# Optimization experiments

Hardware: AMD Instinct MI355X
Metric: run time of the kernel (lower is better)

The kernel has to match this reference:

```python
import jax, jax.numpy as jnp
import numpy as np

HIDDEN = 256


def setup_inputs() -> dict:
    key = jax.random.key(0)
    ks = jax.random.split(key, 16)
    bs, T, wv, vocab, inp = 256, 256, 100, 600, 64
    s = 0.05
    lengths = jax.random.randint(ks[2], (bs,), 2, T + 1)
    lengths = lengths.at[0].set(T)  # ensure max(decoder_length) == T-1
    return {
        "encoder_out": jax.random.normal(ks[0], (bs, inp), jnp.float32),
        "encoded_captions": jax.random.normal(ks[1], (bs, T, wv), jnp.float32),
        "w_ih": jax.random.normal(ks[3], (4 * HIDDEN, inp), jnp.float32) * s,
        "w_hh": jax.random.normal(ks[4], (4 * HIDDEN, HIDDEN), jnp.float32) * s,
        "b_ih": jax.random.normal(ks[5], (4 * HIDDEN,), jnp.float32) * s,
        "b_hh": jax.random.normal(ks[6], (4 * HIDDEN,), jnp.float32) * s,
        "W_out": jax.random.normal(ks[7], (vocab, HIDDEN), jnp.float32) * s,
        "b_out": jax.random.normal(ks[8], (vocab,), jnp.float32) * s,
        "W_emb": jax.random.normal(ks[9], (inp, wv), jnp.float32) * s,
        "b_emb": jax.random.normal(ks[10], (inp,), jnp.float32) * s,
        "W_h": jax.random.normal(ks[11], (HIDDEN, inp), jnp.float32) * s,
        "b_h": jax.random.normal(ks[12], (HIDDEN,), jnp.float32) * s,
        "W_c": jax.random.normal(ks[13], (HIDDEN, inp), jnp.float32) * s,
        "b_c": jax.random.normal(ks[14], (HIDDEN,), jnp.float32) * s,
        "caption_lengths": lengths,
    }


def reference(encoder_out, encoded_captions, w_ih, w_hh, b_ih, b_hh,
              W_out, b_out, W_emb, b_emb, W_h, b_h, W_c, b_c,
              caption_lengths):
    # sort by descending caption length (as torch.sort(descending=True))
    sort_idx = jnp.argsort(-caption_lengths)
    lengths = caption_lengths[sort_idx]
    enc = encoder_out[sort_idx]                  # [bs, 64]
    caps = encoded_captions[sort_idx]            # [bs, T, 100]

    h0 = enc @ W_h.T + b_h                       # [bs, H]
    c0 = enc @ W_c.T + b_c                       # [bs, H]
    emb = caps @ W_emb.T + b_emb                 # [bs, T, 64]

    dec_len = lengths - 1                        # [bs]
    steps = caps.shape[1] - 1                    # == max(dec_len) by construction
    xs = jnp.swapaxes(emb[:, :steps], 0, 1)      # [steps, bs, 64]
    ts = jnp.arange(steps)

    def step(carry, inp):
        h, c = carry
        x, t = inp
        gates = x @ w_ih.T + b_ih + h @ w_hh.T + b_hh      # [bs, 4H]
        i, f, g, o = jnp.split(gates, 4, axis=-1)           # torch gate order i,f,g,o
        i = jax.nn.sigmoid(i); f = jax.nn.sigmoid(f)
        g = jnp.tanh(g);       o = jax.nn.sigmoid(o)
        c_new = f * c + i * g
        h_new = o * jnp.tanh(c_new)
        active = (t < dec_len)[:, None]                     # shrinking batch == mask (sorted)
        logits = h_new @ W_out.T + b_out                    # [bs, vocab]
        pred = jnp.where(active, logits, jnp.float32(-1.0))
        h = jnp.where(active, h_new, h)
        c = jnp.where(active, c_new, c)
        return (h, c), pred

    (_, _), preds = jax.lax.scan(step, (h0, c0), (xs, ts))
    predicts = jnp.swapaxes(preds, 0, 1)         # [bs, steps, vocab]
    return predicts, caps, dec_len, sort_idx
```

## Files before the change

### kernel.cpp

```cpp
#include <hip/hip_runtime.h>
#include <hip/hip_fp16.h>

#define BS 256
#define T 256
#define STEPS 255
#define WV 100
#define INP 64
#define H 256
#define G4 1024
#define VOCAB 600
#define VT 38

typedef _Float16 f16x2 __attribute__((ext_vector_type(2)));
typedef _Float16 f16x8 __attribute__((ext_vector_type(8)));
typedef float f32x4 __attribute__((ext_vector_type(4)));

__device__ __forceinline__ float fdot2(unsigned w, unsigned h, float acc) {
#if defined(__has_builtin) && __has_builtin(__builtin_amdgcn_fdot2)
    return __builtin_amdgcn_fdot2(__builtin_bit_cast(f16x2, w),
                                  __builtin_bit_cast(f16x2, h), acc, false);
#else
    __half2 wv = *(const __half2*)&w;
    __half2 hv = *(const __half2*)&h;
    float2 wf = __half22float2(wv), hf = __half22float2(hv);
    return acc + wf.x * hf.x + wf.y * hf.y;
#endif
}

__device__ __forceinline__ float quad_reduce(float x) {
    int a = __builtin_bit_cast(int, x);
    int b = __builtin_amdgcn_update_dpp(0, a, 0xB1, 0xF, 0xF, true);
    float s = x + __builtin_bit_cast(float, b);
    int c = __builtin_bit_cast(int, s);
    int d = __builtin_amdgcn_update_dpp(0, c, 0x4E, 0xF, 0xF, true);
    return s + __builtin_bit_cast(float, d);
}

__device__ __forceinline__ f32x4 mfma16(uint4 a, uint4 b, f32x4 c) {
    return __builtin_amdgcn_mfma_f32_16x16x32_f16(
        __builtin_bit_cast(f16x8, a), __builtin_bit_cast(f16x8, b), c, 0, 0, 0);
}

__global__ void k_sort(const int* __restrict__ lens, int* __restrict__ sidx,
                       int* __restrict__ dlen, float* __restrict__ out_dec,
                       float* __restrict__ out_sidx) {
    __shared__ int L[BS];
    int i = threadIdx.x;
    L[i] = lens[i];
    __syncthreads();
    int li = L[i];
    int r = 0;
    for (int j = 0; j < BS; ++j) {
        int lj = L[j];
        r += (lj > li) || (lj == li && j < i);
    }
    sidx[r] = i;
    dlen[r] = li - 1;
    out_sidx[r] = (float)i;
    out_dec[r]  = (float)(li - 1);
}

__global__ void k_gather(const float* __restrict__ cin, const int* __restrict__ sidx,
                         float* __restrict__ cout) {
    int b = blockIdx.x;
    int src = sidx[b];
    const float4* in  = (const float4*)(cin + (size_t)src * T * WV);
    float4* out       = (float4*)(cout + (size_t)b * T * WV);
    for (int i = threadIdx.x; i < T * WV / 4; i += 256) out[i] = in[i];
}

__global__ void k_wcomb(const float* __restrict__ w_ih, const float* __restrict__ W_emb,
                        float* __restrict__ Wc) {
    int idx = blockIdx.x * 256 + threadIdx.x;
    int r = idx / WV, cc = idx % WV;
    float acc = 0.f;
    for (int k = 0; k < INP; ++k) acc += w_ih[r * INP + k] * W_emb[k * WV + cc];
    Wc[idx] = acc;
}

__global__ void k_bcomb(const float* __restrict__ w_ih, const float* __restrict__ b_ih,
                        const float* __restrict__ b_hh, const float* __restrict__ b_emb,
                        float* __restrict__ bc) {
    int r = blockIdx.x * 256 + threadIdx.x;
    float acc = b_ih[r] + b_hh[r];
    for (int k = 0; k < INP; ++k) acc += w_ih[r * INP + k] * b_emb[k];
    bc[r] = acc;
}

__global__ void k_packw(const float* __restrict__ w_hh, __half2* __restrict__ wR) {
    int idx = blockIdx.x * 256 + threadIdx.x;
    wR[idx] = __floats2half2_rn(w_hh[(size_t)idx * 2], w_hh[(size_t)idx * 2 + 1]);
}

__global__ void k_packwo(const float* __restrict__ Wo, __half* __restrict__ woHi,
                         __half* __restrict__ woLo) {
    int idx = blockIdx.x * 256 + threadIdx.x;
    int fi = idx >> 9;
    int l  = (idx >> 3) & 63;
    int j  = idx & 7;
    int vt = fi >> 3, kt = fi & 7;
    int v = vt * 16 + (l & 15);
    int k = kt * 32 + ((l >> 4) << 3) + j;
    float w = (v < VOCAB) ? Wo[(size_t)v * H + k] : 0.f;
    __half hi = __float2half(w);
    __half lo = __float2half(w - __half2float(hi));
    woHi[idx] = hi;
    woLo[idx] = lo;
}

__global__ void k_packcaps(const float* __restrict__ caps, __half* __restrict__ cHi,
                           __half* __restrict__ cLo) {
    int idx = blockIdx.x * 256 + threadIdx.x;
    int k = idx & 127;
    int bt = idx >> 7;
    float v = (k < WV) ? caps[(size_t)bt * WV + k] : 0.f;
    __half hi = __float2half(v);
    cHi[idx] = hi;
    cLo[idx] = __float2half(v - __half2float(hi));
}

__global__ void k_packwc(const float* __restrict__ Wc, __half* __restrict__ wcHi,
                         __half* __restrict__ wcLo) {
    int idx = blockIdx.x * 256 + threadIdx.x;
    int fi = idx >> 9;
    int l  = (idx >> 3) & 63;
    int j  = idx & 7;
    int nt = fi >> 2, kt = fi & 3;
    int n = nt * 16 + (l & 15);
    int k = kt * 32 + ((l >> 4) << 3) + j;
    float w = (k < WV) ? Wc[(size_t)n * WV + k] : 0.f;
    __half hi = __float2half(w);
    wcHi[idx] = hi;
    wcLo[idx] = __float2half(w - __half2float(hi));
}

__global__ void k_inithc(const float* __restrict__ enc, const int* __restrict__ sidx,
                         const float* __restrict__ W_h, const float* __restrict__ b_h,
                         const float* __restrict__ W_c, const float* __restrict__ b_c,
                         float* __restrict__ h_st, float* __restrict__ c_st) {
    int b = blockIdx.x, j = threadIdx.x;
    __shared__ __align__(16) float e[INP];
    int src = sidx[b];
    if (j < INP) e[j] = enc[src * INP + j];
    __syncthreads();
    const float4* e4  = (const float4*)e;
    const float4* wh4 = (const float4*)(W_h + (size_t)j * INP);
    const float4* wc4 = (const float4*)(W_c + (size_t)j * INP);
    float ah = b_h[j], ac = b_c[j];
    #pragma unroll
    for (int k4 = 0; k4 < INP / 4; ++k4) {
        float4 ev = e4[k4];
        float4 wh = wh4[k4];
        float4 wc = wc4[k4];
        ah += ev.x * wh.x + ev.y * wh.y + ev.z * wh.z + ev.w * wh.w;
        ac += ev.x * wc.x + ev.y * wc.y + ev.z * wc.z + ev.w * wc.w;
    }
    h_st[b * H + j] = ah;
    c_st[b * H + j] = ac;
}

__global__ __launch_bounds__(256) void k_xg(const __half* __restrict__ cHi,
        const __half* __restrict__ cLo, const __half* __restrict__ wcHi,
        const __half* __restrict__ wcLo, const float* __restrict__ bc,
        const int* __restrict__ dlen, float* __restrict__ xg, int t0, int Cc) {
    int b = blockIdx.y;
    int ct0 = blockIdx.x * 32;
    if (t0 + ct0 >= dlen[b]) return;
    int tid = threadIdx.x;
    int l = tid & 63, wid = tid >> 6;
    int lhi = l >> 4, llo = l & 15;

    uint4 aH[2][4], aL[2][4];
    #pragma unroll
    for (int m = 0; m < 2; ++m) {
        int rr = ct0 + m * 16 + llo;
        if (rr >= Cc) rr = Cc - 1;
        size_t base = ((size_t)b * T + (t0 + rr)) * 128 + lhi * 8;
        #pragma unroll
        for (int kt = 0; kt < 4; ++kt) {
            aH[m][kt] = *(const uint4*)(cHi + base + kt * 32);
            aL[m][kt] = *(const uint4*)(cLo + base + kt * 32);
        }
    }
    const uint4* bh4 = (const uint4*)wcHi;
    const uint4* bl4 = (const uint4*)wcLo;
    for (int i = 0; i < 16; ++i) {
        int nt = wid * 16 + i;
        float bias = bc[nt * 16 + llo];
        f32x4 acc0 = {bias, bias, bias, bias};
        f32x4 acc1 = acc0;
        #pragma unroll
        for (int kt = 0; kt < 4; ++kt) {
            uint4 bh = bh4[(nt * 4 + kt) * 64 + l];
            uint4 bl = bl4[(nt * 4 + kt) * 64 + l];
            acc0 = mfma16(aH[0][kt], bh, acc0);
            acc1 = mfma16(aH[1][kt], bh, acc1);
            acc0 = mfma16(aH[0][kt], bl, acc0);
            acc1 = mfma16(aH[1][kt], bl, acc1);
            acc0 = mfma16(aL[0][kt], bh, acc0);
            acc1 = mfma16(aL[1][kt], bh, acc1);
        }
        #pragma unroll
        for (int m = 0; m < 2; ++m) {
            f32x4 A = m ? acc1 : acc0;
            #pragma unroll
            for (int ii = 0; ii < 4; ++ii) {
                int rr = ct0 + m * 16 + lhi * 4 + ii;
                if (rr < Cc)
                    xg[((size_t)b * Cc + rr) * G4 + nt * 16 + llo] = A[ii];
            }
        }
    }
}

#define LSTM_SMEM (131072 + 2 * 1152)

__global__ __launch_bounds__(512)
__attribute__((amdgpu_waves_per_eu(2, 2)))
void k_lstm(const __half2* __restrict__ wR,
        const float* __restrict__ xg, const int* __restrict__ dlen,
        float* __restrict__ h_st, float* __restrict__ c_st,
        __half* __restrict__ hck, int t0, int Cc) {
    extern __shared__ __align__(16) char smem[];
    uint4*    wl4  = (uint4*)smem;
    unsigned* hbuf = (unsigned*)(smem + 131072);

    int b = blockIdx.x, tid = threadIdx.x;
    int steps_b = dlen[b];
    if (t0 >= steps_b) return;

    int lane = tid & 63;
    int q = lane & 3;
    int Q = tid >> 2;
    int rx = 2 * Q + (q & 1);

    const uint4* wR4 = (const uint4*)wR;

    uint4 wreg[6][8];
    #pragma unroll
    for (int j = 0; j < 6; ++j) {
        int grow = (j >> 1) * 256 + 2 * Q + (j & 1);
        #pragma unroll
        for (int u = 0; u < 8; ++u)
            wreg[j][u] = wR4[grow * 32 + q * 8 + u];
    }
    #pragma unroll
    for (int s = 0; s < 2; ++s)
        #pragma unroll
        for (int u = 0; u < 8; ++u)
            wl4[((u * 2 + s) * 128 + Q) * 4 + q] =
                wR4[(768 + 2 * Q + s) * 32 + q * 8 + u];

    float c = c_st[b * H + rx];
    float hcur = h_st[b * H + rx];
    {
        __half hh16 = __float2half(hcur);
        __half hl16 = __float2half(hcur - __half2float(hh16));
        if (q < 2) {
            int hidx = (rx >> 6) * 72 + (rx & 63);
            ((__half*)(hbuf))[hidx] = hh16;
            ((__half*)(hbuf + 144))[hidx] = hl16;
        }
    }
    __syncthreads();

    int tend = t0 + Cc; if (tend > steps_b) tend = steps_b;
    const float* xgp = xg + (size_t)b * Cc * G4;
    __half* hckp = hck + (size_t)b * Cc * H;
    int p = 0;

    for (int t = t0; t < tend; ++t) {
        float xi = xgp[rx];
        float xf = xgp[256 + rx];
        float xgg = xgp[512 + rx];
        float xo = xgp[768 + rx];

        const uint4* hh4 = (const uint4*)(hbuf + p * 288);
        const uint4* hl4 = (const uint4*)(hbuf + p * 288 + 144);

        float ah[8], al[8];
        #pragma unroll
        for (int j = 0; j < 8; ++j) { ah[j] = 0.f; al[j] = 0.f; }

        #pragma unroll
        for (int u = 0; u < 8; ++u) {
            uint4 hh = hh4[q * 9 + u];
            uint4 hl = hl4[q * 9 + u];
            #pragma unroll
            for (int j = 0; j < 6; ++j) {
                uint4 w = wreg[j][u];
                ah[j] = fdot2(w.x, hh.x, ah[j]);
                ah[j] = fdot2(w.y, hh.y, ah[j]);
                ah[j] = fdot2(w.z, hh.z, ah[j]);
                ah[j] = fdot2(w.w, hh.w, ah[j]);
                al[j] = fdot2(w.x, hl.x, al[j]);
                al[j] = fdot2(w.y, hl.y, al[j]);
                al[j] = fdot2(w.z, hl.z, al[j]);
                al[j] = fdot2(w.w, hl.w, al[j]);
            }
            uint4 w6 = wl4[((u * 2 + 0) * 128 + Q) * 4 + q];
            uint4 w7 = wl4[((u * 2 + 1) * 128 + Q) * 4 + q];
            ah[6] = fdot2(w6.x, hh.x, ah[6]);
            ah[6] = fdot2(w6.y, hh.y, ah[6]);
            ah[6] = fdot2(w6.z, hh.z, ah[6]);
            ah[6] = fdot2(w6.w, hh.w, ah[6]);
            al[6] = fdot2(w6.x, hl.x, al[6]);
            al[6] = fdot2(w6.y, hl.y, al[6]);
            al[6] = fdot2(w6.z, hl.z, al[6]);
            al[6] = fdot2(w6.w, hl.w, al[6]);
            ah[7] = fdot2(w7.x, hh.x, ah[7]);
            ah[7] = fdot2(w7.y, hh.y, ah[7]);
            ah[7] = fdot2(w7.z, hh.z, ah[7]);
            ah[7] = fdot2(w7.w, hh.w, ah[7]);
            al[7] = fdot2(w7.x, hl.x, al[7]);
            al[7] = fdot2(w7.y, hl.y, al[7]);
            al[7] = fdot2(w7.z, hl.z, al[7]);
            al[7] = fdot2(w7.w, hl.w, al[7]);
        }

        float tt[8];
        #pragma unroll
        for (int j = 0; j < 8; ++j) tt[j] = quad_reduce(ah[j] + al[j]);

        int odd = q & 1;
        float pi = odd ? tt[1] : tt[0];
        float pf = odd ? tt[3] : tt[2];
        float pg = odd ? tt[5] : tt[4];
        float po = odd ? tt[7] : tt[6];
        float iv = 1.f / (1.f + __expf(-(pi + xi)));
        float fv = 1.f / (1.f + __expf(-(pf + xf)));
        float gv = tanhf(pg + xgg);
        float ov = 1.f / (1.f + __expf(-(po + xo)));
        c = fv * c + iv * gv;
        float nh = ov * tanhf(c);
        hcur = nh;
        __half hh16 = __float2half(nh);
        __half hl16 = __float2half(nh - __half2float(hh16));
        if (q < 2) {
            hckp[rx] = hh16;
            int hidx = (rx >> 6) * 72 + (rx & 63);
            ((__half*)(hbuf + (p ^ 1) * 288))[hidx] = hh16;
            ((__half*)(hbuf + (p ^ 1) * 288 + 144))[hidx] = hl16;
        }
        __syncthreads();
        p ^= 1;
        xgp += G4;
        hckp += H;
    }
    if (q < 2) { h_st[b * H + rx] = hcur; c_st[b * H + rx] = c; }
}

__global__ __launch_bounds__(64) void k_logits(const __half* __restrict__ hck,
        const __half* __restrict__ woHi, const __half* __restrict__ woLo,
        const float* __restrict__ bo, const int* __restrict__ dlen,
        float* __restrict__ pred, int t0, int Cc) {
    int b = blockIdx.y;
    int ct0 = blockIdx.x * 32;
    if (ct0 >= Cc) return;
    int steps_b = dlen[b];
    int l = threadIdx.x;
    int lhi = l >> 4, llo = l & 15;

    if (t0 + ct0 >= steps_b) {
        for (int r = 0; r < 32; ++r) {
            int t = t0 + ct0 + r;
            if (r >= Cc - ct0 || t >= STEPS) break;
            float* pr = pred + ((size_t)b * STEPS + t) * VOCAB;
            for (int v = l; v < VOCAB; v += 64) pr[v] = -1.f;
        }
        return;
    }

    uint4 a[2][8];
    #pragma unroll
    for (int m = 0; m < 2; ++m) {
        int rr = ct0 + m * 16 + llo;
        int rc = (rr < Cc) ? rr : (Cc - 1);
        const uint4* rp = (const uint4*)(hck + ((size_t)b * Cc + rc) * H);
        #pragma unroll
        for (int kt = 0; kt < 8; ++kt) a[m][kt] = rp[kt * 4 + lhi];
    }

    const uint4* bh4 = (const uint4*)woHi;
    const uint4* bl4 = (const uint4*)woLo;
    for (int vt = 0; vt < VT; ++vt) {
        int v = vt * 16 + llo;
        float bias = (v < VOCAB) ? bo[v] : 0.f;
        f32x4 acc0 = {bias, bias, bias, bias};
        f32x4 acc1 = acc0;
        #pragma unroll
        for (int kt = 0; kt < 8; ++kt) {
            uint4 bh = bh4[(vt * 8 + kt) * 64 + l];
            acc0 = mfma16(a[0][kt], bh, acc0);
            acc1 = mfma16(a[1][kt], bh, acc1);
        }
        #pragma unroll
        for (int kt = 0; kt < 8; ++kt) {
            uint4 bl = bl4[(vt * 8 + kt) * 64 + l];
            acc0 = mfma16(a[0][kt], bl, acc0);
            acc1 = mfma16(a[1][kt], bl, acc1);
        }
        if (v < VOCAB) {
            #pragma unroll
            for (int m = 0; m < 2; ++m) {
                f32x4 A = m ? acc1 : acc0;
                #pragma unroll
                for (int i = 0; i < 4; ++i) {
                    int r = ct0 + m * 16 + lhi * 4 + i;
                    int t = t0 + r;
                    if (r < Cc && t < STEPS)
                        pred[((size_t)b * STEPS + t) * VOCAB + v] =
                            (t < steps_b) ? A[i] : -1.f;
                }
            }
        }
    }
}

extern "C" void kernel_launch(void* const* d_in, const int* in_sizes, int n_in,
                              void* d_out, int out_size, void* d_ws, size_t ws_size,
                              hipStream_t stream) {
    const float* enc   = (const float*)d_in[0];
    const float* caps  = (const float*)d_in[1];
    const float* w_ih  = (const float*)d_in[2];
    const float* w_hh  = (const float*)d_in[3];
    const float* b_ih  = (const float*)d_in[4];
    const float* b_hh  = (const float*)d_in[5];
    const float* W_out = (const float*)d_in[6];
    const float* b_out = (const float*)d_in[7];
    const float* W_emb = (const float*)d_in[8];
    const float* b_emb = (const float*)d_in[9];
    const float* W_h   = (const float*)d_in[10];
    const float* b_h   = (const float*)d_in[11];
    const float* W_c   = (const float*)d_in[12];
    const float* b_c   = (const float*)d_in[13];
    const int*   lens  = (const int*)d_in[14];

    float* out_pred = (float*)d_out;
    float* out_caps = out_pred + (size_t)BS * STEPS * VOCAB;
    float* out_dec  = out_caps + (size_t)BS * T * WV;
    float* out_sidx = out_dec + BS;

    char* w = (char*)d_ws;
    size_t off = 0;
    auto take = [&](size_t bytes) -> char* {
        char* p = w + off;
        off += (bytes + 255) & ~(size_t)255;
        return p;
    };
    int*     sidx = (int*)take(BS * 4);
    int*     dlen = (int*)take(BS * 4);
    float*   Wc   = (float*)take((size_t)G4 * WV * 4);
    float*   bc   = (float*)take(G4 * 4);
    float*   h_st = (float*)take((size_t)BS * H * 4);
    float*   c_st = (float*)take((size_t)BS * H * 4);
    __half2* wR   = (__half2*)take((size_t)G4 * (H / 2) * 4);
    __half*  woHi = (__half*)take((size_t)VT * 8 * 64 * 8 * 2);
    __half*  woLo = (__half*)take((size_t)VT * 8 * 64 * 8 * 2);
    __half*  cHi  = (__half*)take((size_t)BS * T * 128 * 2);
    __half*  cLo  = (__half*)take((size_t)BS * T * 128 * 2);
    __half*  wcHi = (__half*)take((size_t)64 * 4 * 64 * 8 * 2);
    __half*  wcLo = (__half*)take((size_t)64 * 4 * 64 * 8 * 2);

    size_t rem = (ws_size > off) ? (ws_size - off) : 0;
    size_t per_step = (size_t)BS * G4 * 4 + (size_t)BS * H * 2 + 1024;
    int C = (int)(rem / per_step);
    if (C < 1) C = 1;
    if (C > STEPS) C = STEPS;
    float*  xg  = (float*)take((size_t)BS * C * G4 * 4);
    __half* hck = (__half*)take((size_t)BS * C * H * 2);

    (void)hipFuncSetAttribute((const void*)k_lstm,
                              hipFuncAttributeMaxDynamicSharedMemorySize, LSTM_SMEM);

    k_sort<<<1, 256, 0, stream>>>(lens, sidx, dlen, out_dec, out_sidx);
    k_gather<<<BS, 256, 0, stream>>>(caps, sidx, out_caps);
    k_wcomb<<<G4 * WV / 256, 256, 0, stream>>>(w_ih, W_emb, Wc);
    k_bcomb<<<G4 / 256, 256, 0, stream>>>(w_ih, b_ih, b_hh, b_emb, bc);
    k_packw<<<G4 * (H / 2) / 256, 256, 0, stream>>>(w_hh, wR);
    k_packwo<<<VT * 8 * 64 * 8 / 256, 256, 0, stream>>>(W_out, woHi, woLo);
    k_packcaps<<<BS * T * 128 / 256, 256, 0, stream>>>(out_caps, cHi, cLo);
    k_packwc<<<64 * 4 * 64 * 8 / 256, 256, 0, stream>>>(Wc, wcHi, wcLo);
    k_inithc<<<BS, 256, 0, stream>>>(enc, sidx, W_h, b_h, W_c, b_c, h_st, c_st);

    for (int t0 = 0; t0 < STEPS; t0 += C) {
        int Cc = STEPS - t0; if (Cc > C) Cc = C;
        dim3 gx((Cc + 31) / 32, BS);
        k_xg<<<gx, 256, 0, stream>>>(cHi, cLo, wcHi, wcLo, bc, dlen, xg, t0, Cc);
        k_lstm<<<BS, 512, LSTM_SMEM, stream>>>(wR, xg, dlen, h_st, c_st, hck, t0, Cc);
        k_logits<<<gx, 64, 0, stream>>>(hck, woHi, woLo, b_out, dlen, out_pred, t0, Cc);
    }
}
```

Baseline: 1.284 ms.

## Stream last two W_hh row groups from global/L2 instead of LDS

Drops the 128 KB LDS copy of the output-gate weight rows in the LSTM kernel. Those rows are now read each step from a pre-packed global buffer that is coalesced for the access pattern and shared through L2 by all blocks. A new pack kernel builds this buffer, and the step barrier becomes an explicit lgkmcnt wait plus s_barrier with a sched_barrier. The intent is to cut LDS footprint and the per-block LDS fill. The cost is a global-memory load latency inside every serial recurrence step.

After: 1.580 ms. 1.23x slower.

```diff
diff --git a/kernel.cpp b/kernel.cpp
--- a/kernel.cpp
+++ b/kernel.cpp
@@ -90,6 +90,12 @@
 __global__ void k_packw(const float* __restrict__ w_hh, __half2* __restrict__ wR) {
     int idx = blockIdx.x * 256 + threadIdx.x;
     wR[idx] = __floats2half2_rn(w_hh[(size_t)idx * 2], w_hh[(size_t)idx * 2 + 1]);
+}
+
+__global__ void k_packo(const __half2* __restrict__ wR, uint4* __restrict__ woq) {
+    int idx = blockIdx.x * 256 + threadIdx.x;
+    int q = idx & 3, Q = (idx >> 2) & 127, s = (idx >> 9) & 1, u = idx >> 10;
+    woq[idx] = ((const uint4*)wR)[(768 + 2 * Q + s) * 32 + q * 8 + u];
 }
 
 __global__ void k_packwo(const float* __restrict__ Wo, __half* __restrict__ woHi,
@@ -213,17 +219,16 @@
     }
 }
 
-#define LSTM_SMEM (131072 + 2 * 1152)
+#define LSTM_SMEM (2 * 1152)
 
 __global__ __launch_bounds__(512)
 __attribute__((amdgpu_waves_per_eu(2, 2)))
-void k_lstm(const __half2* __restrict__ wR,
+void k_lstm(const __half2* __restrict__ wR, const uint4* __restrict__ woq,
         const float* __restrict__ xg, const int* __restrict__ dlen,
         float* __restrict__ h_st, float* __restrict__ c_st,
         __half* __restrict__ hck, int t0, int Cc) {
     extern __shared__ __align__(16) char smem[];
-    uint4*    wl4  = (uint4*)smem;
-    unsigned* hbuf = (unsigned*)(smem + 131072);
+    unsigned* hbuf = (unsigned*)smem;
 
     int b = blockIdx.x, tid = threadIdx.x;
     int steps_b = dlen[b];
@@ -244,12 +249,6 @@
         for (int u = 0; u < 8; ++u)
             wreg[j][u] = wR4[grow * 32 + q * 8 + u];
     }
-    #pragma unroll
-    for (int s = 0; s < 2; ++s)
-        #pragma unroll
-        for (int u = 0; u < 8; ++u)
-            wl4[((u * 2 + s) * 128 + Q) * 4 + q] =
-                wR4[(768 + 2 * Q + s) * 32 + q * 8 + u];
 
     float c = c_st[b * H + rx];
     float hcur = h_st[b * H + rx];
@@ -267,6 +266,7 @@
     int tend = t0 + Cc; if (tend > steps_b) tend = steps_b;
     const float* xgp = xg + (size_t)b * Cc * G4;
     __half* hckp = hck + (size_t)b * Cc * H;
+    const uint4* wq = woq + Q * 4 + q;
     int p = 0;
 
     for (int t = t0; t < tend; ++t) {
@@ -298,8 +298,8 @@
                 al[j] = fdot2(w.z, hl.z, al[j]);
                 al[j] = fdot2(w.w, hl.w, al[j]);
             }
-            uint4 w6 = wl4[((u * 2 + 0) * 128 + Q) * 4 + q];
-            uint4 w7 = wl4[((u * 2 + 1) * 128 + Q) * 4 + q];
+            uint4 w6 = wq[(u * 2 + 0) * 512];
+            uint4 w7 = wq[(u * 2 + 1) * 512];
             ah[6] = fdot2(w6.x, hh.x, ah[6]);
             ah[6] = fdot2(w6.y, hh.y, ah[6]);
             ah[6] = fdot2(w6.z, hh.z, ah[6]);
@@ -342,7 +342,8 @@
             ((__half*)(hbuf + (p ^ 1) * 288))[hidx] = hh16;
             ((__half*)(hbuf + (p ^ 1) * 288 + 144))[hidx] = hl16;
         }
-        __syncthreads();
+        asm volatile("s_waitcnt lgkmcnt(0)\n\ts_barrier" ::: "memory");
+        __builtin_amdgcn_sched_barrier(0);
         p ^= 1;
         xgp += G4;
         hckp += H;
@@ -455,6 +456,7 @@
     float*   h_st = (float*)take((size_t)BS * H * 4);
     float*   c_st = (float*)take((size_t)BS * H * 4);
     __half2* wR   = (__half2*)take((size_t)G4 * (H / 2) * 4);
+    uint4*   woq  = (uint4*)take((size_t)8192 * 16);
     __half*  woHi = (__half*)take((size_t)VT * 8 * 64 * 8 * 2);
     __half*  woLo = (__half*)take((size_t)VT * 8 * 64 * 8 * 2);
     __half*  cHi  = (__half*)take((size_t)BS * T * 128 * 2);
@@ -478,6 +480,7 @@
     k_wcomb<<<G4 * WV / 256, 256, 0, stream>>>(w_ih, W_emb, Wc);
     k_bcomb<<<G4 / 256, 256, 0, stream>>>(w_ih, b_ih, b_hh, b_emb, bc);
     k_packw<<<G4 * (H / 2) / 256, 256, 0, stream>>>(w_hh, wR);
+    k_packo<<<8192 / 256, 256, 0, stream>>>(wR, woq);
     k_packwo<<<VT * 8 * 64 * 8 / 256, 256, 0, stream>>>(W_out, woHi, woLo);
     k_packcaps<<<BS * T * 128 / 256, 256, 0, stream>>>(out_caps, cHi, cLo);
     k_packwc<<<64 * 4 * 64 * 8 / 256, 256, 0, stream>>>(Wc, wcHi, wcLo);
@@ -487,7 +490,7 @@
         int Cc = STEPS - t0; if (Cc > C) Cc = C;
         dim3 gx((Cc + 31) / 32, BS);
         k_xg<<<gx, 256, 0, stream>>>(cHi, cLo, wcHi, wcLo, bc, dlen, xg, t0, Cc);
-        k_lstm<<<BS, 512, LSTM_SMEM, stream>>>(wR, xg, dlen, h_st, c_st, hck, t0, Cc);
+        k_lstm<<<BS, 512, LSTM_SMEM, stream>>>(wR, woq, xg, dlen, h_st, c_st, hck, t0, Cc);
         k_logits<<<gx, 64, 0, stream>>>(hck, woHi, woLo, b_out, dlen, out_pred, t0, Cc);
     }
 }
```
